# Performance work log

Hardware: AMD Instinct MI355X
Metric: run time of the kernel (lower is better)

Reference implementation:

```python
import jax, jax.numpy as jnp
import numpy as np

D_MODEL = 1024
M = 50
B, N = 8, 4096
NOISE_P = 0.0464
TEMP = 0.1
EPS = 1e-12


def _l2norm(v):
    return v / jnp.clip(jnp.linalg.norm(v, axis=-1, keepdims=True), EPS)


def setup_inputs() -> dict:
    key = jax.random.key(0)
    ks = jax.random.split(key, 8)
    x = jax.random.normal(ks[0], (B, N, D_MODEL), dtype=jnp.float32)
    prime_nodes = jax.random.normal(ks[1], (M, D_MODEL), dtype=jnp.float32)
    w_cov = jnp.float32(1.0)
    w_hyd = jnp.float32(0.5)
    w_vdw = jnp.float32(0.1)
    A_cov = jnp.asarray(np.roll(np.eye(M, dtype=np.float32), 1, axis=0))
    A_hyd = jnp.asarray(np.tril(np.ones((M, M), dtype=np.float32), k=-1))
    A_vdw = jax.random.normal(ks[2], (M, M), dtype=jnp.float32) * 0.05
    # expert MLP: Linear(D,4D) -> GELU -> Linear(4D,D); kaiming-uniform-ish init
    lim1 = 1.0 / np.sqrt(D_MODEL)
    lim2 = 1.0 / np.sqrt(4 * D_MODEL)
    W1 = jax.random.uniform(ks[3], (D_MODEL, 4 * D_MODEL), minval=-lim1, maxval=lim1, dtype=jnp.float32)
    b1 = jax.random.uniform(ks[4], (4 * D_MODEL,), minval=-lim1, maxval=lim1, dtype=jnp.float32)
    W2 = jax.random.uniform(ks[5], (4 * D_MODEL, D_MODEL), minval=-lim2, maxval=lim2, dtype=jnp.float32)
    b2 = jax.random.uniform(ks[6], (D_MODEL,), minval=-lim2, maxval=lim2, dtype=jnp.float32)
    return {"x": x, "prime_nodes": prime_nodes, "w_cov": w_cov, "w_hyd": w_hyd,
            "w_vdw": w_vdw, "A_cov": A_cov, "A_hyd": A_hyd, "A_vdw": A_vdw,
            "W1": W1, "b1": b1, "W2": W2, "b2": b2}


def reference(x, prime_nodes, w_cov, w_hyd, w_vdw, A_cov, A_hyd, A_vdw, W1, b1, W2, b2):
    # soft codebook routing: cosine-sim softmax over M primes, temperature 0.1
    C = jax.nn.softmax(jnp.einsum('bnd,md->bnm', _l2norm(x), _l2norm(prime_nodes)) / TEMP, axis=-1)
    H_prime = jnp.einsum('bnm,bnd->bmd', C, x)  # (B, M, D)
    A = jax.nn.softmax(w_cov * A_cov + w_hyd * A_hyd + w_vdw * A_vdw, axis=-1)
    # einsum('mn,bmd->bmd', A, H_prime): n only appears in A -> rowsum scaling
    H = A.sum(axis=1)[None, :, None] * H_prime
    # single latent step (latent_steps=1 default)
    U, _, Vt = jnp.linalg.svd(H, full_matrices=False)  # U:(B,M,M), Vt:(B,M,D)
    H_logic = jnp.einsum('bij,bjd->bid', U, Vt)  # orthogonal (polar) factor
    nk1, nk2 = jax.random.split(jax.random.key(42))
    mask = (jax.random.uniform(nk1, H_logic.shape) < NOISE_P).astype(H_logic.dtype)
    noise = jax.random.normal(nk2, H_logic.shape, dtype=H_logic.dtype) * 0.1
    z = H_logic + mask * noise
    h = jax.nn.gelu(z @ W1 + b1, approximate=False)
    H = jnp.tanh(h @ W2 + b2)
    # residual decode back to tokens (continuous_mode=False)
    return x + jnp.einsum('bnm,bmd->bnd', C, H)
```

## Files before the change

### kernel.cpp

```cpp
#include <hip/hip_runtime.h>
#include <stdint.h>
#include <math.h>

#define NS_ITERS 26
#define PIT 72
#define P2  72

typedef unsigned short u16;
typedef __attribute__((ext_vector_type(8))) short short8;
typedef __attribute__((ext_vector_type(4))) float f32x4;

__device__ __forceinline__ u16 f2b(float f){
  unsigned u = __float_as_uint(f);
  unsigned r = (u + 0x7FFFu + ((u>>16)&1u)) >> 16;
  return (u16)r;
}
__device__ __forceinline__ float b2f(u16 h){ return __uint_as_float(((unsigned)h)<<16); }
__device__ __forceinline__ unsigned pk2(float lo, float hi){
  return (unsigned)f2b(lo) | ((unsigned)f2b(hi) << 16);
}

__host__ __device__ constexpr uint32_t rotl32(uint32_t v, int n){ return (v<<n)|(v>>(32-n)); }
struct TFOut { uint32_t a, b; };
__host__ __device__ constexpr TFOut tf2x32(uint32_t k0, uint32_t k1, uint32_t x0, uint32_t x1){
  uint32_t ks2 = k0 ^ k1 ^ 0x1BD11BDAu;
  x0 += k0; x1 += k1;
#define TFR(R) x0 += x1; x1 = rotl32(x1,(R)) ^ x0;
  TFR(13) TFR(15) TFR(26) TFR(6)
  x0 += k1; x1 += ks2 + 1u;
  TFR(17) TFR(29) TFR(16) TFR(24)
  x0 += ks2; x1 += k0 + 2u;
  TFR(13) TFR(15) TFR(26) TFR(6)
  x0 += k0; x1 += k1 + 3u;
  TFR(17) TFR(29) TFR(16) TFR(24)
  x0 += k1; x1 += ks2 + 4u;
  TFR(13) TFR(15) TFR(26) TFR(6)
  x0 += ks2; x1 += k0 + 5u;
#undef TFR
  return TFOut{x0, x1};
}

__device__ __forceinline__ float erfinv_f32(float x){
  float w = -log1pf(-x*x);
  float p;
  if (w < 5.0f) {
    w -= 2.5f;
    p = 2.81022636e-08f;
    p = fmaf(p, w, 3.43273939e-07f);
    p = fmaf(p, w, -3.5233877e-06f);
    p = fmaf(p, w, -4.39150654e-06f);
    p = fmaf(p, w, 0.00021858087f);
    p = fmaf(p, w, -0.00125372503f);
    p = fmaf(p, w, -0.00417768164f);
    p = fmaf(p, w, 0.246640727f);
    p = fmaf(p, w, 1.50140941f);
  } else {
    w = sqrtf(w) - 3.0f;
    p = -0.000200214257f;
    p = fmaf(p, w, 0.000100950558f);
    p = fmaf(p, w, 0.00134934322f);
    p = fmaf(p, w, -0.00367342844f);
    p = fmaf(p, w, 0.00573950773f);
    p = fmaf(p, w, -0.0076224613f);
    p = fmaf(p, w, 0.00943887047f);
    p = fmaf(p, w, 1.00167406f);
    p = fmaf(p, w, 2.83297682f);
  }
  return p * x;
}

__global__ __launch_bounds__(256) void kprepAll(const float* __restrict__ prime, u16* __restrict__ PT,
                                                const float* __restrict__ W1, u16* __restrict__ W1T,
                                                const float* __restrict__ W2, u16* __restrict__ W2T){
  int blk = blockIdx.x;
  int tid = threadIdx.x;
  if (blk < 64){
    int m = blk;
    u16* dst = PT + m*1024;
    if (m >= 50){ for (int k = tid; k < 1024; k += 256) dst[k] = 0; return; }
    __shared__ float red[256];
    const float* pr = prime + m*1024;
    float ss = 0.f;
    for (int k = tid; k < 1024; k += 256){ float v = pr[k]; ss = fmaf(v,v,ss); }
    red[tid] = ss; __syncthreads();
    for (int s = 128; s > 0; s >>= 1){ if (tid < s) red[tid] += red[tid+s]; __syncthreads(); }
    float sc = 1.0f / fmaxf(sqrtf(red[0]), 1e-12f);
    for (int k = tid; k < 1024; k += 256) dst[k] = f2b(pr[k]*sc);
    return;
  }
  const float* src; u16* dst; int srcStride, dstStride;
  if (blk < 1088){
    int t = blk - 64;
    int kt2 = t >> 6, nt2 = t & 63;
    src = W1 + (size_t)(kt2*64)*4096 + nt2*64; srcStride = 4096;
    dst = W1T + (size_t)(nt2*64)*1024 + kt2*64; dstStride = 1024;
  } else {
    int t = blk - 1088;
    int kt2 = t >> 4, dt2 = t & 15;
    src = W2 + (size_t)(kt2*64)*1024 + dt2*64; srcStride = 1024;
    dst = W2T + (size_t)(dt2*64)*4096 + kt2*64; dstStride = 4096;
  }
  __shared__ __align__(16) u16 ts[64*PIT];
  int r = tid>>2, sseg = tid&3;
  {
    const float* s0 = src + (size_t)r*srcStride + sseg*16;
    unsigned p[8];
#pragma unroll
    for (int i = 0; i < 4; i++){
      float4 v = *reinterpret_cast<const float4*>(s0 + i*4);
      p[2*i]   = pk2(v.x, v.y);
      p[2*i+1] = pk2(v.z, v.w);
    }
    uint4 w0; w0.x=p[0]; w0.y=p[1]; w0.z=p[2]; w0.w=p[3];
    uint4 w1; w1.x=p[4]; w1.y=p[5]; w1.z=p[6]; w1.w=p[7];
    *reinterpret_cast<uint4*>(&ts[r*PIT + sseg*16])     = w0;
    *reinterpret_cast<uint4*>(&ts[r*PIT + sseg*16 + 8]) = w1;
  }
  __syncthreads();
  {
    int n2 = tid>>2, kseg = tid&3;
    unsigned q[8];
#pragma unroll
    for (int j = 0; j < 8; j++){
      u16 lo = ts[(kseg*16 + 2*j)*PIT + n2];
      u16 hi = ts[(kseg*16 + 2*j+1)*PIT + n2];
      q[j] = (unsigned)lo | ((unsigned)hi<<16);
    }
    u16* d2 = dst + (size_t)n2*dstStride + kseg*16;
    uint4 w0; w0.x=q[0]; w0.y=q[1]; w0.z=q[2]; w0.w=q[3];
    uint4 w1; w1.x=q[4]; w1.y=q[5]; w1.z=q[6]; w1.w=q[7];
    *reinterpret_cast<uint4*>(d2)   = w0;
    *reinterpret_cast<uint4*>(d2+8) = w1;
  }
}

__global__ __launch_bounds__(256) void kC(const float* __restrict__ x, const u16* __restrict__ PT,
                                          u16* __restrict__ C, u16* __restrict__ CT){
  int blk = blockIdx.x; int b = blk>>6, n0 = (blk&63)<<6;
  int tid = threadIdx.x, lane = tid&63, w = tid>>6;
  __shared__ __align__(16) u16 xs[2][64*PIT];
  __shared__ __align__(16) u16 ps[2][64*PIT];
  __shared__ float sqn[64];
  f32x4 acc[4] = {{0,0,0,0},{0,0,0,0},{0,0,0,0},{0,0,0,0}};
  float sqa = 0.f;
  int stok = tid>>2, sseg = tid&3;
  const float* xb = x + ((size_t)(b*4096 + n0))*1024;
  for (int kc = 0; kc < 16; kc++){
    int k0 = kc*64, cb = kc & 1;
    {
      const float* src = xb + (size_t)stok*1024 + k0 + sseg*16;
      unsigned p[8];
#pragma unroll
      for (int i = 0; i < 4; i++){
        float4 v = *reinterpret_cast<const float4*>(src + i*4);
        sqa = fmaf(v.x,v.x,sqa); sqa = fmaf(v.y,v.y,sqa);
        sqa = fmaf(v.z,v.z,sqa); sqa = fmaf(v.w,v.w,sqa);
        p[2*i]   = pk2(v.x, v.y);
        p[2*i+1] = pk2(v.z, v.w);
      }
      uint4 w0; w0.x=p[0]; w0.y=p[1]; w0.z=p[2]; w0.w=p[3];
      uint4 w1; w1.x=p[4]; w1.y=p[5]; w1.z=p[6]; w1.w=p[7];
      *reinterpret_cast<uint4*>(&xs[cb][stok*PIT + sseg*16])     = w0;
      *reinterpret_cast<uint4*>(&xs[cb][stok*PIT + sseg*16 + 8]) = w1;
    }
    {
      const u16* src = PT + (size_t)stok*1024 + k0 + sseg*16;
      *reinterpret_cast<uint4*>(&ps[cb][stok*PIT + sseg*16])   = *reinterpret_cast<const uint4*>(src);
      *reinterpret_cast<uint4*>(&ps[cb][stok*PIT + sseg*16+8]) = *reinterpret_cast<const uint4*>(src+8);
    }
    __syncthreads();
#pragma unroll
    for (int s = 0; s < 2; s++){
      short8 a = *reinterpret_cast<const short8*>(&xs[cb][(16*w + (lane&15))*PIT + s*32 + (lane>>4)*8]);
#pragma unroll
      for (int t = 0; t < 4; t++){
        short8 bb = *reinterpret_cast<const short8*>(&ps[cb][(t*16 + (lane&15))*PIT + s*32 + (lane>>4)*8]);
        acc[t] = __builtin_amdgcn_mfma_f32_16x16x32_bf16(a, bb, acc[t], 0, 0, 0);
      }
    }
  }
  sqa += __shfl_xor(sqa, 1, 64);
  sqa += __shfl_xor(sqa, 2, 64);
  if ((tid & 3) == 0) sqn[stok] = 10.0f / fmaxf(sqrtf(sqa), 1e-12f);
  __syncthreads();
  u16* cl = xs[0];
#pragma unroll
  for (int r = 0; r < 4; r++){
    int gt = 16*w + (lane>>4)*4 + r;
    float scale = sqn[gt];
    float v[4];
#pragma unroll
    for (int t = 0; t < 4; t++) v[t] = acc[t][r] * scale;
    if ((lane&15) >= 2) v[3] = -1e30f;
    float mx = fmaxf(fmaxf(v[0],v[1]), fmaxf(v[2],v[3]));
#pragma unroll
    for (int off = 1; off < 16; off <<= 1) mx = fmaxf(mx, __shfl_xor(mx, off, 64));
    float e[4], sum = 0.f;
#pragma unroll
    for (int t = 0; t < 4; t++){ e[t] = __expf(v[t]-mx); sum += e[t]; }
#pragma unroll
    for (int off = 1; off < 16; off <<= 1) sum += __shfl_xor(sum, off, 64);
    float inv = 1.0f / sum;
#pragma unroll
    for (int t = 0; t < 4; t++) cl[gt*PIT + t*16 + (lane&15)] = f2b(e[t]*inv);
  }
  __syncthreads();
  {
    u16* dst = C + ((size_t)(b*4096 + n0 + stok))*64 + sseg*16;
    *reinterpret_cast<uint4*>(dst)   = *reinterpret_cast<const uint4*>(&cl[stok*PIT + sseg*16]);
    *reinterpret_cast<uint4*>(dst+8) = *reinterpret_cast<const uint4*>(&cl[stok*PIT + sseg*16+8]);
  }
  {
    int m = tid>>2, nseg = tid&3;
    unsigned vs[8];
#pragma unroll
    for (int j = 0; j < 8; j++){
      u16 lo = cl[(nseg*16 + 2*j)*PIT + m];
      u16 hi = cl[(nseg*16 + 2*j+1)*PIT + m];
      vs[j] = (unsigned)lo | ((unsigned)hi<<16);
    }
    u16* dst = CT + ((size_t)(b*64 + m))*4096 + n0 + nseg*16;
    uint4 w0; w0.x=vs[0]; w0.y=vs[1]; w0.z=vs[2]; w0.w=vs[3];
    uint4 w1; w1.x=vs[4]; w1.y=vs[5]; w1.z=vs[6]; w1.w=vs[7];
    *reinterpret_cast<uint4*>(dst)   = w0;
    *reinterpret_cast<uint4*>(dst+8) = w1;
  }
}

__global__ __launch_bounds__(256) void kHp2(const float* __restrict__ x, const u16* __restrict__ CT,
                                            float* __restrict__ Hpart){
  int blk = blockIdx.x;
  int kt = blk & 3, dt = (blk >> 2) & 15, b = blk >> 6;
  int d0 = dt*64;
  int tid = threadIdx.x, lane = tid&63, w = tid>>6;
  __shared__ __align__(16) u16 cs[2][64*PIT];
  __shared__ __align__(16) u16 xt[2][64*PIT];
  f32x4 acc[4] = {{0,0,0,0},{0,0,0,0},{0,0,0,0},{0,0,0,0}};
  int nn = tid>>2, seg = tid&3;
  int np = tid & 31, dsg = tid >> 5;
  for (int nc = 0; nc < 16; nc++){
    int n0 = kt*1024 + nc*64, cb = nc & 1;
    {
      const u16* src = CT + ((size_t)(b*64 + nn))*4096 + n0 + seg*16;
      *reinterpret_cast<uint4*>(&cs[cb][nn*PIT + seg*16])   = *reinterpret_cast<const uint4*>(src);
      *reinterpret_cast<uint4*>(&cs[cb][nn*PIT + seg*16+8]) = *reinterpret_cast<const uint4*>(src+8);
    }
    {
      const float* s0 = x + ((size_t)(b*4096 + n0 + 2*np))*1024 + d0 + dsg*8;
      const float* s1 = s0 + 1024;
      float4 a0 = *reinterpret_cast<const float4*>(s0);
      float4 a1 = *reinterpret_cast<const float4*>(s0+4);
      float4 c0v = *reinterpret_cast<const float4*>(s1);
      float4 c1v = *reinterpret_cast<const float4*>(s1+4);
      float av[8] = {a0.x,a0.y,a0.z,a0.w,a1.x,a1.y,a1.z,a1.w};
      float cv[8] = {c0v.x,c0v.y,c0v.z,c0v.w,c1v.x,c1v.y,c1v.z,c1v.w};
#pragma unroll
      for (int j2 = 0; j2 < 8; j2++){
        int dd = dsg*8 + j2;
        *reinterpret_cast<unsigned*>(&xt[cb][dd*PIT + 2*np]) = pk2(av[j2], cv[j2]);
      }
    }
    __syncthreads();
#pragma unroll
    for (int s = 0; s < 2; s++){
      short8 a = *reinterpret_cast<const short8*>(&cs[cb][(16*w + (lane&15))*PIT + s*32 + (lane>>4)*8]);
#pragma unroll
      for (int t = 0; t < 4; t++){
        short8 bb = *reinterpret_cast<const short8*>(&xt[cb][(t*16 + (lane&15))*PIT + s*32 + (lane>>4)*8]);
        acc[t] = __builtin_amdgcn_mfma_f32_16x16x32_bf16(a, bb, acc[t], 0, 0, 0);
      }
    }
  }
#pragma unroll
  for (int t = 0; t < 4; t++)
#pragma unroll
    for (int r = 0; r < 4; r++){
      int m = 16*w + (lane>>4)*4 + r;
      int d = d0 + t*16 + (lane&15);
      if (m < 50) Hpart[(((size_t)(b*4) + kt)*50 + m)*1024 + d] = acc[t][r];
    }
}

__global__ void kredH(const float* __restrict__ Hpart, float* __restrict__ H, u16* __restrict__ Hb){
  int e = blockIdx.x*256 + threadIdx.x;
  int b = e >> 16, rem = e & 65535;
  int m = rem >> 10, d = rem & 1023;
  size_t o = ((size_t)(b*64 + m))*1024 + d;
  if (m < 50){
    const float* p = Hpart + (size_t)b*204800 + m*1024 + d;
    float s = p[0] + p[51200] + p[102400] + p[153600];
    H[o] = s;
    Hb[o] = f2b(s);
  } else {
    Hb[o] = 0;
  }
}

__global__ __launch_bounds__(256) void kgram(const u16* __restrict__ Hb, float* __restrict__ G){
  int b = blockIdx.x;
  int tid = threadIdx.x, lane = tid&63, w = tid>>6;
  __shared__ __align__(16) u16 hs[64*PIT];
  f32x4 acc[4] = {{0,0,0,0},{0,0,0,0},{0,0,0,0},{0,0,0,0}};
  int m = tid>>2, seg = tid&3;
  for (int kc = 0; kc < 16; kc++){
    int k0 = kc*64;
    __syncthreads();
    const u16* src = Hb + ((size_t)(b*64 + m))*1024 + k0 + seg*16;
    *reinterpret_cast<uint4*>(&hs[m*PIT + seg*16])   = *reinterpret_cast<const uint4*>(src);
    *reinterpret_cast<uint4*>(&hs[m*PIT + seg*16+8]) = *reinterpret_cast<const uint4*>(src+8);
    __syncthreads();
#pragma unroll
    for (int s = 0; s < 2; s++){
      short8 a = *reinterpret_cast<const short8*>(&hs[(16*w + (lane&15))*PIT + s*32 + (lane>>4)*8]);
#pragma unroll
      for (int t = 0; t < 4; t++){
        short8 bb = *reinterpret_cast<const short8*>(&hs[(t*16 + (lane&15))*PIT + s*32 + (lane>>4)*8]);
        acc[t] = __builtin_amdgcn_mfma_f32_16x16x32_bf16(a, bb, acc[t], 0, 0, 0);
      }
    }
  }
#pragma unroll
  for (int t = 0; t < 4; t++)
#pragma unroll
    for (int r = 0; r < 4; r++){
      int i = 16*w + (lane>>4)*4 + r;
      int j = t*16 + (lane&15);
      if (i < 50 && j < 50) G[(size_t)b*2500 + i*50 + j] = acc[t][r];
    }
}

__global__ __launch_bounds__(256) void kns3(const float* __restrict__ G, float* __restrict__ Wm){
  int b = blockIdx.x;
  __shared__ __align__(16) u16 Yr[2][64*P2], Yc[2][64*P2], Zr[2][64*P2], Zc[2][64*P2];
  __shared__ __align__(16) u16 Tr[64*P2], Tc[64*P2];
  __shared__ float sv[2];
  int tid = threadIdx.x, lane = tid&63, w = tid>>6;
  int lr = lane>>4, lc = lane&15;
  int row0 = 16*w;
  const float* Gb = G + (size_t)b*2500;
  if (tid < 64){
    float v = (tid < 50) ? Gb[tid*50+tid] : 0.f;
    for (int off = 1; off < 64; off <<= 1) v += __shfl_xor(v, off, 64);
    if (tid == 0){ sv[0] = 1.0f / v; sv[1] = rsqrtf(v); }
  }
  __syncthreads();
  float rs = sv[0];
  for (int idx = tid; idx < 4096; idx += 256){
    int r = idx>>6, c = idx&63;
    float yv = (r<50 && c<50) ? Gb[r*50+c]*rs : ((r==c) ? 1.f : 0.f);
    float zv = (r==c) ? 1.f : 0.f;
    u16 yb = f2b(yv), zb = f2b(zv);
    Yr[0][r*P2+c] = yb; Yc[0][c*P2+r] = yb;
    Zr[0][r*P2+c] = zb; Zc[0][c*P2+r] = zb;
  }
  __syncthreads();
  for (int it = 0; it < NS_ITERS; it++){
    int cur = it & 1, nxt = cur ^ 1;
    {
      short8 a0 = *reinterpret_cast<const short8*>(&Zr[cur][(row0+lc)*P2 + lr*8]);
      short8 a1 = *reinterpret_cast<const short8*>(&Zr[cur][(row0+lc)*P2 + 32 + lr*8]);
      f32x4 acc[4] = {{0,0,0,0},{0,0,0,0},{0,0,0,0},{0,0,0,0}};
#pragma unroll
      for (int t = 0; t < 4; t++){
        short8 b0 = *reinterpret_cast<const short8*>(&Yc[cur][(t*16+lc)*P2 + lr*8]);
        short8 b1 = *reinterpret_cast<const short8*>(&Yc[cur][(t*16+lc)*P2 + 32 + lr*8]);
        acc[t] = __builtin_amdgcn_mfma_f32_16x16x32_bf16(a0, b0, acc[t], 0, 0, 0);
        acc[t] = __builtin_amdgcn_mfma_f32_16x16x32_bf16(a1, b1, acc[t], 0, 0, 0);
      }
#pragma unroll
      for (int t = 0; t < 4; t++)
#pragma unroll
        for (int r = 0; r < 4; r++){
          int row = row0 + lr*4 + r, col = t*16 + lc;
          float v = ((row==col) ? 1.5f : 0.f) - 0.5f*acc[t][r];
          u16 h = f2b(v);
          Tr[row*P2+col] = h; Tc[col*P2+row] = h;
        }
    }
    __syncthreads();
    {
      short8 ya0 = *reinterpret_cast<const short8*>(&Yr[cur][(row0+lc)*P2 + lr*8]);
      short8 ya1 = *reinterpret_cast<const short8*>(&Yr[cur][(row0+lc)*P2 + 32 + lr*8]);
      short8 ta0 = *reinterpret_cast<const short8*>(&Tr[(row0+lc)*P2 + lr*8]);
      short8 ta1 = *reinterpret_cast<const short8*>(&Tr[(row0+lc)*P2 + 32 + lr*8]);
      f32x4 accY[4] = {{0,0,0,0},{0,0,0,0},{0,0,0,0},{0,0,0,0}};
      f32x4 accZ[4] = {{0,0,0,0},{0,0,0,0},{0,0,0,0},{0,0,0,0}};
#pragma unroll
      for (int t = 0; t < 4; t++){
        short8 tb0 = *reinterpret_cast<const short8*>(&Tc[(t*16+lc)*P2 + lr*8]);
        short8 tb1 = *reinterpret_cast<const short8*>(&Tc[(t*16+lc)*P2 + 32 + lr*8]);
        accY[t] = __builtin_amdgcn_mfma_f32_16x16x32_bf16(ya0, tb0, accY[t], 0, 0, 0);
        accY[t] = __builtin_amdgcn_mfma_f32_16x16x32_bf16(ya1, tb1, accY[t], 0, 0, 0);
        short8 zb0 = *reinterpret_cast<const short8*>(&Zc[cur][(t*16+lc)*P2 + lr*8]);
        short8 zb1 = *reinterpret_cast<const short8*>(&Zc[cur][(t*16+lc)*P2 + 32 + lr*8]);
        accZ[t] = __builtin_amdgcn_mfma_f32_16x16x32_bf16(ta0, zb0, accZ[t], 0, 0, 0);
        accZ[t] = __builtin_amdgcn_mfma_f32_16x16x32_bf16(ta1, zb1, accZ[t], 0, 0, 0);
      }
#pragma unroll
      for (int t = 0; t < 4; t++)
#pragma unroll
        for (int r = 0; r < 4; r++){
          int row = row0 + lr*4 + r, col = t*16 + lc;
          u16 hy = f2b(accY[t][r]);
          u16 hz = f2b(accZ[t][r]);
          Yr[nxt][row*P2+col] = hy; Yc[nxt][col*P2+row] = hy;
          Zr[nxt][row*P2+col] = hz; Zc[nxt][col*P2+row] = hz;
        }
    }
    __syncthreads();
  }
  float rss = sv[1];
  int fin = NS_ITERS & 1;
  for (int idx = tid; idx < 2500; idx += 256){
    int r = idx/50, c = idx - r*50;
    Wm[(size_t)b*2500 + idx] = b2f(Zr[fin][r*P2+c]) * rss;
  }
}

__global__ __launch_bounds__(256) void kapply2(const float* __restrict__ H, const float* __restrict__ Wm,
                                               u16* __restrict__ zb){
  TFOut K1 = tf2x32(0u, 42u, 0u, 0u);
  TFOut K2 = tf2x32(0u, 42u, 0u, 1u);
  int blk = blockIdx.x;
  int dt = blk & 15, b = blk >> 4;
  int d0 = dt*64;
  int tid = threadIdx.x;
  int d = tid & 63, mg = tid >> 6;
  __shared__ __align__(16) float WsT[50*64];
  __shared__ float Hs[50*65];
  for (int idx = tid; idx < 3200; idx += 256){
    int j = idx >> 6, c = idx & 63;
    WsT[idx] = (c < 50) ? Wm[(size_t)b*2500 + c*50 + j] : 0.f;
  }
  for (int idx = tid; idx < 3200; idx += 256){
    int j = idx >> 6, c = idx & 63;
    Hs[j*65 + c] = H[((size_t)(b*64) + j)*1024 + d0 + c];
  }
  __syncthreads();
  float acc[16];
#pragma unroll
  for (int i = 0; i < 16; i++) acc[i] = 0.f;
  for (int j = 0; j < 50; j++){
    float hv = Hs[j*65 + d];
    const float* wb = WsT + j*64 + (mg << 4);
#pragma unroll
    for (int q = 0; q < 4; q++){
      float4 wv = *reinterpret_cast<const float4*>(wb + q*4);
      acc[q*4+0] = fmaf(wv.x, hv, acc[q*4+0]);
      acc[q*4+1] = fmaf(wv.y, hv, acc[q*4+1]);
      acc[q*4+2] = fmaf(wv.z, hv, acc[q*4+2]);
      acc[q*4+3] = fmaf(wv.w, hv, acc[q*4+3]);
    }
  }
#pragma unroll
  for (int i = 0; i < 16; i++){
    int m = (mg << 4) + i;
    size_t zo = ((size_t)(b*64 + m))*1024 + d0 + d;
    u16 ov = 0;
    if (m < 50){
      float val = acc[i];
      uint32_t j = (uint32_t)(((b*50 + m) << 10) + d0 + d);
      TFOut r1 = tf2x32(K1.a, K1.b, 0u, j);
      uint32_t bits = r1.a ^ r1.b;
      float u = __uint_as_float(0x3F800000u | (bits >> 9)) - 1.0f;
      if (u < 0.0464f){
        TFOut r2 = tf2x32(K2.a, K2.b, 0u, j);
        uint32_t nb = r2.a ^ r2.b;
        float ww = __uint_as_float(0x3F800000u | (nb >> 9)) - 1.0f;
        const float lo = -0.99999994f;
        float un = fmaxf(lo, fmaf(ww, 2.0f, lo));
        val += 0.1f * (1.4142135f * erfinv_f32(un));
      }
      ov = f2b(val);
    }
    zb[zo] = ov;
  }
}

__global__ __launch_bounds__(256) void kmlp1(const u16* __restrict__ ZbB, const u16* __restrict__ W1T,
                                             const float* __restrict__ b1, u16* __restrict__ Hh){
  int blk = blockIdx.x; int b = blk>>6, c0 = (blk&63)<<6;
  int tid = threadIdx.x, lane = tid&63, w = tid>>6;
  __shared__ __align__(16) u16 az[2][64*PIT];
  __shared__ __align__(16) u16 wt[2][64*PIT];
  f32x4 acc[4] = {{0,0,0,0},{0,0,0,0},{0,0,0,0},{0,0,0,0}};
  int rr = tid>>2, seg = tid&3;
  for (int kc = 0; kc < 16; kc++){
    int k0 = kc*64, cb = kc & 1;
    {
      const u16* src = ZbB + ((size_t)(b*64 + rr))*1024 + k0 + seg*16;
      *reinterpret_cast<uint4*>(&az[cb][rr*PIT + seg*16])   = *reinterpret_cast<const uint4*>(src);
      *reinterpret_cast<uint4*>(&az[cb][rr*PIT + seg*16+8]) = *reinterpret_cast<const uint4*>(src+8);
    }
    {
      const u16* src = W1T + ((size_t)(c0 + rr))*1024 + k0 + seg*16;
      *reinterpret_cast<uint4*>(&wt[cb][rr*PIT + seg*16])   = *reinterpret_cast<const uint4*>(src);
      *reinterpret_cast<uint4*>(&wt[cb][rr*PIT + seg*16+8]) = *reinterpret_cast<const uint4*>(src+8);
    }
    __syncthreads();
#pragma unroll
    for (int s = 0; s < 2; s++){
      short8 a = *reinterpret_cast<const short8*>(&az[cb][(16*w + (lane&15))*PIT + s*32 + (lane>>4)*8]);
#pragma unroll
      for (int t = 0; t < 4; t++){
        short8 bb = *reinterpret_cast<const short8*>(&wt[cb][(t*16 + (lane&15))*PIT + s*32 + (lane>>4)*8]);
        acc[t] = __builtin_amdgcn_mfma_f32_16x16x32_bf16(a, bb, acc[t], 0, 0, 0);
      }
    }
  }
#pragma unroll
  for (int t = 0; t < 4; t++)
#pragma unroll
    for (int r = 0; r < 4; r++){
      int m = 16*w + (lane>>4)*4 + r;
      int n = c0 + t*16 + (lane&15);
      float val = acc[t][r] + b1[n];
      float g = 0.5f * val * (1.0f + erff(val * 0.70710678f));
      Hh[((size_t)(b*64 + m))*4096 + n] = (m < 50) ? f2b(g) : (u16)0;
    }
}

__global__ __launch_bounds__(256) void kmlp2p(const u16* __restrict__ Hh, const u16* __restrict__ W2T,
                                              float* __restrict__ Mpart){
  int blk = blockIdx.x;
  int kt = blk & 3, dt = (blk >> 2) & 15, b = blk >> 6;
  int d0 = dt*64;
  int tid = threadIdx.x, lane = tid&63, w = tid>>6;
  __shared__ __align__(16) u16 az[2][64*PIT];
  __shared__ __align__(16) u16 wt[2][64*PIT];
  f32x4 acc[4] = {{0,0,0,0},{0,0,0,0},{0,0,0,0},{0,0,0,0}};
  int rr = tid>>2, seg = tid&3;
  for (int kc = 0; kc < 16; kc++){
    int k0 = kt*1024 + kc*64, cb = kc & 1;
    {
      const u16* src = Hh + ((size_t)(b*64 + rr))*4096 + k0 + seg*16;
      *reinterpret_cast<uint4*>(&az[cb][rr*PIT + seg*16])   = *reinterpret_cast<const uint4*>(src);
      *reinterpret_cast<uint4*>(&az[cb][rr*PIT + seg*16+8]) = *reinterpret_cast<const uint4*>(src+8);
    }
    {
      const u16* src = W2T + ((size_t)(d0 + rr))*4096 + k0 + seg*16;
      *reinterpret_cast<uint4*>(&wt[cb][rr*PIT + seg*16])   = *reinterpret_cast<const uint4*>(src);
      *reinterpret_cast<uint4*>(&wt[cb][rr*PIT + seg*16+8]) = *reinterpret_cast<const uint4*>(src+8);
    }
    __syncthreads();
#pragma unroll
    for (int s = 0; s < 2; s++){
      short8 a = *reinterpret_cast<const short8*>(&az[cb][(16*w + (lane&15))*PIT + s*32 + (lane>>4)*8]);
#pragma unroll
      for (int t = 0; t < 4; t++){
        short8 bb = *reinterpret_cast<const short8*>(&wt[cb][(t*16 + (lane&15))*PIT + s*32 + (lane>>4)*8]);
        acc[t] = __builtin_amdgcn_mfma_f32_16x16x32_bf16(a, bb, acc[t], 0, 0, 0);
      }
    }
  }
#pragma unroll
  for (int t = 0; t < 4; t++)
#pragma unroll
    for (int r = 0; r < 4; r++){
      int m = 16*w + (lane>>4)*4 + r;
      int d = d0 + t*16 + (lane&15);
      if (m < 50) Mpart[(((size_t)(b*4) + kt)*50 + m)*1024 + d] = acc[t][r];
    }
}

__global__ void kredT(const float* __restrict__ Mpart, const float* __restrict__ b2, u16* __restrict__ HfT){
  int e = blockIdx.x*256 + threadIdx.x;
  int b = e >> 16, rem = e & 65535;
  int m = rem >> 10, d = rem & 1023;
  u16 outv = 0;
  if (m < 50){
    const float* p = Mpart + (size_t)b*204800 + m*1024 + d;
    float s = p[0] + p[51200] + p[102400] + p[153600] + b2[d];
    outv = f2b(tanhf(s));
  }
  HfT[((size_t)(b*1024) + d)*64 + m] = outv;
}

__global__ __launch_bounds__(256) void kdec2(const float* __restrict__ x, const u16* __restrict__ C,
                                             const u16* __restrict__ HfT, float* __restrict__ out){
  int blk = blockIdx.x;
  int dq = blk & 3, nt = (blk >> 2) & 63, b = blk >> 8;
  int n0 = nt << 6;
  int tid = threadIdx.x, lane = tid&63, w = tid>>6;
  __shared__ __align__(16) u16 ctile[64*PIT];
  __shared__ __align__(16) u16 htile[64*PIT];
  __shared__ __align__(16) float obuf[64*68];
  int rr = tid>>2, seg = tid&3;
  {
    const u16* src = C + ((size_t)(b*4096 + n0 + rr))*64 + seg*16;
    *reinterpret_cast<uint4*>(&ctile[rr*PIT + seg*16])   = *reinterpret_cast<const uint4*>(src);
    *reinterpret_cast<uint4*>(&ctile[rr*PIT + seg*16+8]) = *reinterpret_cast<const uint4*>(src+8);
  }
  __syncthreads();
  short8 afrag[2];
#pragma unroll
  for (int s = 0; s < 2; s++)
    afrag[s] = *reinterpret_cast<const short8*>(&ctile[(16*w + (lane&15))*PIT + s*32 + (lane>>4)*8]);
  for (int dt2 = 0; dt2 < 4; dt2++){
    int d0 = (dq*4 + dt2) * 64;
    __syncthreads();
    {
      const u16* src = HfT + ((size_t)(b*1024 + d0 + rr))*64 + seg*16;
      *reinterpret_cast<uint4*>(&htile[rr*PIT + seg*16])   = *reinterpret_cast<const uint4*>(src);
      *reinterpret_cast<uint4*>(&htile[rr*PIT + seg*16+8]) = *reinterpret_cast<const uint4*>(src+8);
    }
    __syncthreads();
    f32x4 acc[4] = {{0,0,0,0},{0,0,0,0},{0,0,0,0},{0,0,0,0}};
#pragma unroll
    for (int s = 0; s < 2; s++){
#pragma unroll
      for (int t = 0; t < 4; t++){
        short8 bb = *reinterpret_cast<const short8*>(&htile[(t*16 + (lane&15))*PIT + s*32 + (lane>>4)*8]);
        acc[t] = __builtin_amdgcn_mfma_f32_16x16x32_bf16(afrag[s], bb, acc[t], 0, 0, 0);
      }
    }
#pragma unroll
    for (int t = 0; t < 4; t++)
#pragma unroll
      for (int r = 0; r < 4; r++){
        int nl = 16*w + (lane>>4)*4 + r;
        int dl = t*16 + (lane&15);
        obuf[nl*68 + dl] = acc[t][r];
      }
    __syncthreads();
#pragma unroll
    for (int pass = 0; pass < 4; pass++){
      int s2 = tid + pass*256;
      int nl = s2 >> 4, sg = s2 & 15;
      size_t o = ((size_t)(b*4096 + n0 + nl))*1024 + d0 + sg*4;
      float4 xv = *reinterpret_cast<const float4*>(x + o);
      const float* ob = &obuf[nl*68 + sg*4];
      float4 ov;
      ov.x = xv.x + ob[0];
      ov.y = xv.y + ob[1];
      ov.z = xv.z + ob[2];
      ov.w = xv.w + ob[3];
      *reinterpret_cast<float4*>(out + o) = ov;
    }
  }
}

extern "C" void kernel_launch(void* const* d_in, const int* in_sizes, int n_in,
                              void* d_out, int out_size, void* d_ws, size_t ws_size,
                              hipStream_t stream) {
  (void)in_sizes; (void)n_in; (void)out_size;
  if (ws_size < (size_t)19755264) return;
  const float* x  = (const float*)d_in[0];
  const float* pn = (const float*)d_in[1];
  const float* W1 = (const float*)d_in[8];
  const float* b1 = (const float*)d_in[9];
  const float* W2 = (const float*)d_in[10];
  const float* b2 = (const float*)d_in[11];
  float* out = (float*)d_out;
  char* ws = (char*)d_ws;

  u16*   W1T = (u16*)d_out;
  u16*   W2T = (u16*)d_out + 4194304;

  u16*   C   = (u16*)(ws);
  u16*   CT  = (u16*)(ws + 4194304);
  u16*   ZbB = (u16*)(ws + 4194304 + 1638400);
  u16*   HfT = (u16*)(ws + 4194304 + 2686976);
  u16*   Hh  = (u16*)(ws + 8388608);
  u16*   Hb  = (u16*)(ws + 8388608);
  float* H   = (float*)(ws + 8388608 + 1048576);
  float* HP  = (float*)(ws + 12582912);
  u16*   PT  = (u16*)(ws + 19136512);
  float* G   = (float*)(ws + 19267584);
  float* WM  = (float*)(ws + 19347584);

  hipLaunchKernelGGL(kprepAll, dim3(2112), dim3(256), 0, stream, pn, PT, W1, W1T, W2, W2T);
  hipLaunchKernelGGL(kC,       dim3(512),  dim3(256), 0, stream, x, PT, C, CT);
  hipLaunchKernelGGL(kHp2,     dim3(512),  dim3(256), 0, stream, x, CT, HP);
  hipLaunchKernelGGL(kredH,    dim3(2048), dim3(256), 0, stream, HP, H, Hb);
  hipLaunchKernelGGL(kgram,    dim3(8),    dim3(256), 0, stream, Hb, G);
  hipLaunchKernelGGL(kns3,     dim3(8),    dim3(256), 0, stream, G, WM);
  hipLaunchKernelGGL(kapply2,  dim3(128),  dim3(256), 0, stream, H, WM, ZbB);
  hipLaunchKernelGGL(kmlp1,    dim3(512),  dim3(256), 0, stream, ZbB, W1T, b1, Hh);
  hipLaunchKernelGGL(kmlp2p,   dim3(512),  dim3(256), 0, stream, Hh, W2T, HP);
  hipLaunchKernelGGL(kredT,    dim3(2048), dim3(256), 0, stream, HP, b2, HfT);
  hipLaunchKernelGGL(kdec2,    dim3(2048), dim3(256), 0, stream, x, C, HfT, out);
}
```

Baseline: 231.7 us.

## Fuse Gram and Newton-Schulz kernels, overlap weight transpose with serial NS

Merges the Gram-matrix kernel and the Newton-Schulz iteration kernel into one launch, keeping G in shared memory instead of round-tripping through global. The W1/W2 bf16 transpose work moves out of the first prep kernel into extra blocks of this fused launch (512 blocks, 4 tiles each), so it runs alongside the 8 latency-bound NS blocks that would otherwise leave most CUs idle. An extra barrier was added because the T buffers now alias the G scratch. The cost is higher shared-memory use per block, and the transpose blocks now carry the same large shared footprint, which may cut their occupancy.

```diff
diff --git a/kernel.cpp b/kernel.cpp
--- a/kernel.cpp
+++ b/kernel.cpp
@@ -69,69 +69,19 @@
   return p * x;
 }
 
-__global__ __launch_bounds__(256) void kprepAll(const float* __restrict__ prime, u16* __restrict__ PT,
-                                                const float* __restrict__ W1, u16* __restrict__ W1T,
-                                                const float* __restrict__ W2, u16* __restrict__ W2T){
-  int blk = blockIdx.x;
+__global__ __launch_bounds__(256) void kprep(const float* __restrict__ prime, u16* __restrict__ PT){
+  int m = blockIdx.x;
   int tid = threadIdx.x;
-  if (blk < 64){
-    int m = blk;
-    u16* dst = PT + m*1024;
-    if (m >= 50){ for (int k = tid; k < 1024; k += 256) dst[k] = 0; return; }
-    __shared__ float red[256];
-    const float* pr = prime + m*1024;
-    float ss = 0.f;
-    for (int k = tid; k < 1024; k += 256){ float v = pr[k]; ss = fmaf(v,v,ss); }
-    red[tid] = ss; __syncthreads();
-    for (int s = 128; s > 0; s >>= 1){ if (tid < s) red[tid] += red[tid+s]; __syncthreads(); }
-    float sc = 1.0f / fmaxf(sqrtf(red[0]), 1e-12f);
-    for (int k = tid; k < 1024; k += 256) dst[k] = f2b(pr[k]*sc);
-    return;
-  }
-  const float* src; u16* dst; int srcStride, dstStride;
-  if (blk < 1088){
-    int t = blk - 64;
-    int kt2 = t >> 6, nt2 = t & 63;
-    src = W1 + (size_t)(kt2*64)*4096 + nt2*64; srcStride = 4096;
-    dst = W1T + (size_t)(nt2*64)*1024 + kt2*64; dstStride = 1024;
-  } else {
-    int t = blk - 1088;
-    int kt2 = t >> 4, dt2 = t & 15;
-    src = W2 + (size_t)(kt2*64)*1024 + dt2*64; srcStride = 1024;
-    dst = W2T + (size_t)(dt2*64)*4096 + kt2*64; dstStride = 4096;
-  }
-  __shared__ __align__(16) u16 ts[64*PIT];
-  int r = tid>>2, sseg = tid&3;
-  {
-    const float* s0 = src + (size_t)r*srcStride + sseg*16;
-    unsigned p[8];
-#pragma unroll
-    for (int i = 0; i < 4; i++){
-      float4 v = *reinterpret_cast<const float4*>(s0 + i*4);
-      p[2*i]   = pk2(v.x, v.y);
-      p[2*i+1] = pk2(v.z, v.w);
-    }
-    uint4 w0; w0.x=p[0]; w0.y=p[1]; w0.z=p[2]; w0.w=p[3];
-    uint4 w1; w1.x=p[4]; w1.y=p[5]; w1.z=p[6]; w1.w=p[7];
-    *reinterpret_cast<uint4*>(&ts[r*PIT + sseg*16])     = w0;
-    *reinterpret_cast<uint4*>(&ts[r*PIT + sseg*16 + 8]) = w1;
-  }
-  __syncthreads();
-  {
-    int n2 = tid>>2, kseg = tid&3;
-    unsigned q[8];
-#pragma unroll
-    for (int j = 0; j < 8; j++){
-      u16 lo = ts[(kseg*16 + 2*j)*PIT + n2];
-      u16 hi = ts[(kseg*16 + 2*j+1)*PIT + n2];
-      q[j] = (unsigned)lo | ((unsigned)hi<<16);
-    }
-    u16* d2 = dst + (size_t)n2*dstStride + kseg*16;
-    uint4 w0; w0.x=q[0]; w0.y=q[1]; w0.z=q[2]; w0.w=q[3];
-    uint4 w1; w1.x=q[4]; w1.y=q[5]; w1.z=q[6]; w1.w=q[7];
-    *reinterpret_cast<uint4*>(d2)   = w0;
-    *reinterpret_cast<uint4*>(d2+8) = w1;
-  }
+  u16* dst = PT + m*1024;
+  if (m >= 50){ for (int k = tid; k < 1024; k += 256) dst[k] = 0; return; }
+  __shared__ float red[256];
+  const float* pr = prime + m*1024;
+  float ss = 0.f;
+  for (int k = tid; k < 1024; k += 256){ float v = pr[k]; ss = fmaf(v,v,ss); }
+  red[tid] = ss; __syncthreads();
+  for (int s = 128; s > 0; s >>= 1){ if (tid < s) red[tid] += red[tid+s]; __syncthreads(); }
+  float sc = 1.0f / fmaxf(sqrtf(red[0]), 1e-12f);
+  for (int k = tid; k < 1024; k += 256) dst[k] = f2b(pr[k]*sc);
 }
 
 __global__ __launch_bounds__(256) void kC(const float* __restrict__ x, const u16* __restrict__ PT,
@@ -296,50 +246,102 @@
   }
 }
 
-__global__ __launch_bounds__(256) void kgram(const u16* __restrict__ Hb, float* __restrict__ G){
-  int b = blockIdx.x;
+__global__ __launch_bounds__(256) void kgramNS(const u16* __restrict__ Hb, float* __restrict__ Wm,
+                                               const float* __restrict__ W1, u16* __restrict__ W1T,
+                                               const float* __restrict__ W2, u16* __restrict__ W2T){
+  __shared__ __align__(16) u16 Yr[2][64*P2], Yc[2][64*P2], Zr[2][64*P2], Zc[2][64*P2];
+  __shared__ __align__(16) u16 TrTc[2][64*P2];
+  __shared__ __align__(16) u16 ts[64*PIT];
+  __shared__ float sv[2];
+  int blk = blockIdx.x;
   int tid = threadIdx.x, lane = tid&63, w = tid>>6;
-  __shared__ __align__(16) u16 hs[64*PIT];
-  f32x4 acc[4] = {{0,0,0,0},{0,0,0,0},{0,0,0,0},{0,0,0,0}};
-  int m = tid>>2, seg = tid&3;
-  for (int kc = 0; kc < 16; kc++){
-    int k0 = kc*64;
-    __syncthreads();
-    const u16* src = Hb + ((size_t)(b*64 + m))*1024 + k0 + seg*16;
-    *reinterpret_cast<uint4*>(&hs[m*PIT + seg*16])   = *reinterpret_cast<const uint4*>(src);
-    *reinterpret_cast<uint4*>(&hs[m*PIT + seg*16+8]) = *reinterpret_cast<const uint4*>(src+8);
-    __syncthreads();
-#pragma unroll
-    for (int s = 0; s < 2; s++){
-      short8 a = *reinterpret_cast<const short8*>(&hs[(16*w + (lane&15))*PIT + s*32 + (lane>>4)*8]);
-#pragma unroll
-      for (int t = 0; t < 4; t++){
-        short8 bb = *reinterpret_cast<const short8*>(&hs[(t*16 + (lane&15))*PIT + s*32 + (lane>>4)*8]);
-        acc[t] = __builtin_amdgcn_mfma_f32_16x16x32_bf16(a, bb, acc[t], 0, 0, 0);
-      }
-    }
-  }
-#pragma unroll
-  for (int t = 0; t < 4; t++)
-#pragma unroll
-    for (int r = 0; r < 4; r++){
-      int i = 16*w + (lane>>4)*4 + r;
-      int j = t*16 + (lane&15);
-      if (i < 50 && j < 50) G[(size_t)b*2500 + i*50 + j] = acc[t][r];
-    }
-}
-
-__global__ __launch_bounds__(256) void kns3(const float* __restrict__ G, float* __restrict__ Wm){
-  int b = blockIdx.x;
-  __shared__ __align__(16) u16 Yr[2][64*P2], Yc[2][64*P2], Zr[2][64*P2], Zc[2][64*P2];
-  __shared__ __align__(16) u16 Tr[64*P2], Tc[64*P2];
-  __shared__ float sv[2];
-  int tid = threadIdx.x, lane = tid&63, w = tid>>6;
-  int lr = lane>>4, lc = lane&15;
-  int row0 = 16*w;
-  const float* Gb = G + (size_t)b*2500;
+
+  if (blk >= 8){
+    int tblk = blk - 8;
+    for (int i = 0; i < 4; i++){
+      int g = tblk*4 + i;
+      const float* src; u16* dst; int ss, ds;
+      if (g < 1024){
+        int kt2 = g >> 6, nt2 = g & 63;
+        src = W1 + (size_t)(kt2*64)*4096 + nt2*64; ss = 4096;
+        dst = W1T + (size_t)(nt2*64)*1024 + kt2*64; ds = 1024;
+      } else {
+        int t = g - 1024;
+        int kt2 = t >> 4, dt2 = t & 15;
+        src = W2 + (size_t)(kt2*64)*1024 + dt2*64; ss = 1024;
+        dst = W2T + (size_t)(dt2*64)*4096 + kt2*64; ds = 4096;
+      }
+      int r = tid>>2, sseg = tid&3;
+      __syncthreads();
+      {
+        const float* s0 = src + (size_t)r*ss + sseg*16;
+        unsigned p[8];
+#pragma unroll
+        for (int q = 0; q < 4; q++){
+          float4 v = *reinterpret_cast<const float4*>(s0 + q*4);
+          p[2*q]   = pk2(v.x, v.y);
+          p[2*q+1] = pk2(v.z, v.w);
+        }
+        uint4 w0; w0.x=p[0]; w0.y=p[1]; w0.z=p[2]; w0.w=p[3];
+        uint4 w1; w1.x=p[4]; w1.y=p[5]; w1.z=p[6]; w1.w=p[7];
+        *reinterpret_cast<uint4*>(&ts[r*PIT + sseg*16])     = w0;
+        *reinterpret_cast<uint4*>(&ts[r*PIT + sseg*16 + 8]) = w1;
+      }
+      __syncthreads();
+      {
+        int n2 = tid>>2, kseg = tid&3;
+        unsigned q[8];
+#pragma unroll
+        for (int j = 0; j < 8; j++){
+          u16 lo = ts[(kseg*16 + 2*j)*PIT + n2];
+          u16 hi = ts[(kseg*16 + 2*j+1)*PIT + n2];
+          q[j] = (unsigned)lo | ((unsigned)hi<<16);
+        }
+        u16* d2 = dst + (size_t)n2*ds + kseg*16;
+        uint4 w0; w0.x=q[0]; w0.y=q[1]; w0.z=q[2]; w0.w=q[3];
+        uint4 w1; w1.x=q[4]; w1.y=q[5]; w1.z=q[6]; w1.w=q[7];
+        *reinterpret_cast<uint4*>(d2)   = w0;
+        *reinterpret_cast<uint4*>(d2+8) = w1;
+      }
+    }
+    return;
+  }
+
+  int b = blk;
+  float* Gf = reinterpret_cast<float*>(&TrTc[0][0]);
+  {
+    f32x4 acc[4] = {{0,0,0,0},{0,0,0,0},{0,0,0,0},{0,0,0,0}};
+    int m = tid>>2, seg = tid&3;
+    for (int kc = 0; kc < 16; kc++){
+      int k0 = kc*64;
+      __syncthreads();
+      const u16* src = Hb + ((size_t)(b*64 + m))*1024 + k0 + seg*16;
+      *reinterpret_cast<uint4*>(&ts[m*PIT + seg*16])   = *reinterpret_cast<const uint4*>(src);
+      *reinterpret_cast<uint4*>(&ts[m*PIT + seg*16+8]) = *reinterpret_cast<const uint4*>(src+8);
+      __syncthreads();
+#pragma unroll
+      for (int s = 0; s < 2; s++){
+        short8 a = *reinterpret_cast<const short8*>(&ts[(16*w + (lane&15))*PIT + s*32 + (lane>>4)*8]);
+#pragma unroll
+        for (int t = 0; t < 4; t++){
+          short8 bb = *reinterpret_cast<const short8*>(&ts[(t*16 + (lane&15))*PIT + s*32 + (lane>>4)*8]);
+          acc[t] = __builtin_amdgcn_mfma_f32_16x16x32_bf16(a, bb, acc[t], 0, 0, 0);
+        }
+      }
+    }
+    __syncthreads();
+#pragma unroll
+    for (int t = 0; t < 4; t++)
+#pragma unroll
+      for (int r = 0; r < 4; r++){
+        int i = 16*w + (lane>>4)*4 + r;
+        int j = t*16 + (lane&15);
+        Gf[i*65 + j] = acc[t][r];
+      }
+  }
+  __syncthreads();
   if (tid < 64){
-    float v = (tid < 50) ? Gb[tid*50+tid] : 0.f;
+    float v = (tid < 50) ? Gf[tid*65 + tid] : 0.f;
     for (int off = 1; off < 64; off <<= 1) v += __shfl_xor(v, off, 64);
     if (tid == 0){ sv[0] = 1.0f / v; sv[1] = rsqrtf(v); }
   }
@@ -347,13 +349,17 @@
   float rs = sv[0];
   for (int idx = tid; idx < 4096; idx += 256){
     int r = idx>>6, c = idx&63;
-    float yv = (r<50 && c<50) ? Gb[r*50+c]*rs : ((r==c) ? 1.f : 0.f);
+    float yv = (r<50 && c<50) ? Gf[r*65+c]*rs : ((r==c) ? 1.f : 0.f);
     float zv = (r==c) ? 1.f : 0.f;
     u16 yb = f2b(yv), zb = f2b(zv);
     Yr[0][r*P2+c] = yb; Yc[0][c*P2+r] = yb;
     Zr[0][r*P2+c] = zb; Zc[0][c*P2+r] = zb;
   }
   __syncthreads();
+  u16* Tr = TrTc[0];
+  u16* Tc = TrTc[1];
+  int lr = lane>>4, lc = lane&15;
+  int row0 = 16*w;
   for (int it = 0; it < NS_ITERS; it++){
     int cur = it & 1, nxt = cur ^ 1;
     {
@@ -367,6 +373,7 @@
         acc[t] = __builtin_amdgcn_mfma_f32_16x16x32_bf16(a0, b0, acc[t], 0, 0, 0);
         acc[t] = __builtin_amdgcn_mfma_f32_16x16x32_bf16(a1, b1, acc[t], 0, 0, 0);
       }
+      __syncthreads();
 #pragma unroll
       for (int t = 0; t < 4; t++)
 #pragma unroll
@@ -666,18 +673,16 @@
   float* H   = (float*)(ws + 8388608 + 1048576);
   float* HP  = (float*)(ws + 12582912);
   u16*   PT  = (u16*)(ws + 19136512);
-  float* G   = (float*)(ws + 19267584);
   float* WM  = (float*)(ws + 19347584);
 
-  hipLaunchKernelGGL(kprepAll, dim3(2112), dim3(256), 0, stream, pn, PT, W1, W1T, W2, W2T);
-  hipLaunchKernelGGL(kC,       dim3(512),  dim3(256), 0, stream, x, PT, C, CT);
-  hipLaunchKernelGGL(kHp2,     dim3(512),  dim3(256), 0, stream, x, CT, HP);
-  hipLaunchKernelGGL(kredH,    dim3(2048), dim3(256), 0, stream, HP, H, Hb);
-  hipLaunchKernelGGL(kgram,    dim3(8),    dim3(256), 0, stream, Hb, G);
-  hipLaunchKernelGGL(kns3,     dim3(8),    dim3(256), 0, stream, G, WM);
-  hipLaunchKernelGGL(kapply2,  dim3(128),  dim3(256), 0, stream, H, WM, ZbB);
-  hipLaunchKernelGGL(kmlp1,    dim3(512),  dim3(256), 0, stream, ZbB, W1T, b1, Hh);
-  hipLaunchKernelGGL(kmlp2p,   dim3(512),  dim3(256), 0, stream, Hh, W2T, HP);
-  hipLaunchKernelGGL(kredT,    dim3(2048), dim3(256), 0, stream, HP, b2, HfT);
-  hipLaunchKernelGGL(kdec2,    dim3(2048), dim3(256), 0, stream, x, C, HfT, out);
-}
+  hipLaunchKernelGGL(kprep,   dim3(64),   dim3(256), 0, stream, pn, PT);
+  hipLaunchKernelGGL(kC,      dim3(512),  dim3(256), 0, stream, x, PT, C, CT);
+  hipLaunchKernelGGL(kHp2,    dim3(512),  dim3(256), 0, stream, x, CT, HP);
+  hipLaunchKernelGGL(kredH,   dim3(2048), dim3(256), 0, stream, HP, H, Hb);
+  hipLaunchKernelGGL(kgramNS, dim3(520),  dim3(256), 0, stream, Hb, WM, W1, W1T, W2, W2T);
+  hipLaunchKernelGGL(kapply2, dim3(128),  dim3(256), 0, stream, H, WM, ZbB);
+  hipLaunchKernelGGL(kmlp1,   dim3(512),  dim3(256), 0, stream, ZbB, W1T, b1, Hh);
+  hipLaunchKernelGGL(kmlp2p,  dim3(512),  dim3(256), 0, stream, Hh, W2T, HP);
+  hipLaunchKernelGGL(kredT,   dim3(2048), dim3(256), 0, stream, HP, b2, HfT);
+  hipLaunchKernelGGL(kdec2,   dim3(2048), dim3(256), 0, stream, x, C, HfT, out);
+}
```

Measured after the change: 220.8 us. 4.7% less time.
